# Kernel tuning notes

Measured on AMD Instinct MI355X. Metric: run time of the kernel, lower is better.

The kernel has to match this reference:

```python
import jax, jax.numpy as jnp
import numpy as np

IN_FEATURES = 4096
OUT_FEATURES = 4096
NUM_FRAGMENTS = 32
FRAGMENT_SIZE = IN_FEATURES // NUM_FRAGMENTS  # 128
COMPRESSED = 512
BATCH = 8192


def setup_inputs() -> dict:
    key = jax.random.key(0)
    k_x, k_sel, k_exp, k_c1, k_c2 = jax.random.split(key, 5)
    inv_sqrt_fs = 1.0 / np.sqrt(FRAGMENT_SIZE)
    return {
        "x": jax.random.normal(k_x, (BATCH, IN_FEATURES), dtype=jnp.float32),
        "selector_weights": jax.random.normal(k_sel, (NUM_FRAGMENTS, FRAGMENT_SIZE), dtype=jnp.float32) * inv_sqrt_fs,
        "expert_weights": jax.random.normal(k_exp, (NUM_FRAGMENTS, FRAGMENT_SIZE, OUT_FEATURES), dtype=jnp.float32) * inv_sqrt_fs,
        # store Linear weights as [in, out] so forward is x @ W
        "w_compressor": jax.random.normal(k_c1, (IN_FEATURES, COMPRESSED), dtype=jnp.float32) * (1.0 / np.sqrt(IN_FEATURES)),
        "w_compressed": jax.random.normal(k_c2, (COMPRESSED, OUT_FEATURES), dtype=jnp.float32) * (1.0 / np.sqrt(COMPRESSED)),
    }


def reference(x, selector_weights, expert_weights, w_compressor, w_compressed):
    B, D = x.shape
    F, S = selector_weights.shape  # num_fragments, fragment_size
    x_frag = x.reshape(B, F, S)
    # selector scores and soft routing probs over fragments
    scores = jnp.einsum('bfi,fi->bf', x_frag, selector_weights)
    probs = jax.nn.softmax(scores, axis=1)  # [B, F]
    # soft-routed expert output: weight fragments by probs first to avoid a [B,F,O] intermediate
    x_weighted = x_frag * probs[:, :, None]  # [B, F, S]
    expert_out = jnp.einsum('bfi,fio->bo', x_weighted, expert_weights)  # [B, O]
    # fragment mask mapped to full feature dim: mask = 1 - probs[fragment_mapping]
    mask = 1.0 - jnp.repeat(probs, S, axis=1)  # [B, D]
    masked_input = x * mask
    compressed_out = (masked_input @ w_compressor) @ w_compressed  # [B, O]
    return expert_out + compressed_out
```

## Files before the change

### kernel.cpp

```cpp
#include <hip/hip_runtime.h>
#include <hip/hip_bf16.h>
#include <stdint.h>

#define BATCH 8192
#define IN_F  4096
#define OUT_F 4096
#define NFRAG 32
#define FSIZE 128
#define COMP  512
#define KCAT  4608

typedef float f32x4 __attribute__((ext_vector_type(4)));
typedef short bf16x8 __attribute__((ext_vector_type(8)));

__device__ __forceinline__ unsigned short f2bf(float f) {
  union { float f; unsigned u; } v; v.f = f;
  return (unsigned short)((v.u + 0x7FFFu + ((v.u >> 16) & 1u)) >> 16);
}
__device__ __forceinline__ unsigned pack2(float a, float b) {
  return (unsigned)f2bf(a) | ((unsigned)f2bf(b) << 16);
}

typedef const __attribute__((address_space(1))) unsigned* as1_u32p;
typedef __attribute__((address_space(3))) unsigned* as3_u32p;

__device__ __forceinline__ void lds_load16(const void* g, void* l) {
  __builtin_amdgcn_global_load_lds((as1_u32p)(uintptr_t)g, (as3_u32p)(uintptr_t)l, 16, 0, 0);
}

__global__ __launch_bounds__(256) void k_route(
    const float* __restrict__ x, const float* __restrict__ sel,
    unsigned short* __restrict__ xw, unsigned short* __restrict__ xm) {
  __shared__ float red[256];
  __shared__ float sc[NFRAG];
  const int b = blockIdx.x;
  const int t = threadIdx.x;
  const float* xr = x + (size_t)b * IN_F;
  const int frag = t >> 3;

  float4 v0 = *(const float4*)&xr[t * 16 + 0];
  float4 v1 = *(const float4*)&xr[t * 16 + 4];
  float4 v2 = *(const float4*)&xr[t * 16 + 8];
  float4 v3 = *(const float4*)&xr[t * 16 + 12];
  const float* sw = sel + frag * FSIZE + (t & 7) * 16;
  float4 s0 = *(const float4*)&sw[0];
  float4 s1 = *(const float4*)&sw[4];
  float4 s2 = *(const float4*)&sw[8];
  float4 s3 = *(const float4*)&sw[12];
  float d = v0.x*s0.x + v0.y*s0.y + v0.z*s0.z + v0.w*s0.w
          + v1.x*s1.x + v1.y*s1.y + v1.z*s1.z + v1.w*s1.w
          + v2.x*s2.x + v2.y*s2.y + v2.z*s2.z + v2.w*s2.w
          + v3.x*s3.x + v3.y*s3.y + v3.z*s3.z + v3.w*s3.w;
  red[t] = d;
  __syncthreads();
  if (t < NFRAG) {
    float s = 0.f;
#pragma unroll
    for (int j = 0; j < 8; ++j) s += red[t * 8 + j];
    sc[t] = s;
  }
  __syncthreads();
  float mx = sc[0];
#pragma unroll
  for (int f = 1; f < NFRAG; ++f) mx = fmaxf(mx, sc[f]);
  float den = 0.f;
#pragma unroll
  for (int f = 0; f < NFRAG; ++f) den += __expf(sc[f] - mx);
  const float p = __expf(sc[frag] - mx) / den;
  const float q = 1.f - p;

  const size_t bw = (size_t)b * KCAT + (size_t)t * 16;
  const size_t bm_ = (size_t)b * IN_F + (size_t)t * 16;
  uint4 w;
  w.x = pack2(v0.x*p, v0.y*p); w.y = pack2(v0.z*p, v0.w*p);
  w.z = pack2(v1.x*p, v1.y*p); w.w = pack2(v1.z*p, v1.w*p);
  *(uint4*)&xw[bw] = w;
  w.x = pack2(v2.x*p, v2.y*p); w.y = pack2(v2.z*p, v2.w*p);
  w.z = pack2(v3.x*p, v3.y*p); w.w = pack2(v3.z*p, v3.w*p);
  *(uint4*)&xw[bw + 8] = w;
  w.x = pack2(v0.x*q, v0.y*q); w.y = pack2(v0.z*q, v0.w*q);
  w.z = pack2(v1.x*q, v1.y*q); w.w = pack2(v1.z*q, v1.w*q);
  *(uint4*)&xm[bm_] = w;
  w.x = pack2(v2.x*q, v2.y*q); w.y = pack2(v2.z*q, v2.w*q);
  w.z = pack2(v3.x*q, v3.y*q); w.w = pack2(v3.z*q, v3.w*q);
  *(uint4*)&xm[bm_ + 8] = w;
}

__global__ __launch_bounds__(256) void k_transpose_bf16(
    const float* __restrict__ src, unsigned short* __restrict__ dst,
    int R, int C, int ldd) {
  __shared__ float tile[64][65];
  const int t = threadIdx.x;
  const int c0 = blockIdx.x * 64, r0 = blockIdx.y * 64;
#pragma unroll
  for (int i = 0; i < 4; ++i) {
    const int q = i * 256 + t;
    const int row = q >> 4;
    const int col = (q & 15) << 2;
    float4 v = *(const float4*)&src[(size_t)(r0 + row) * C + c0 + col];
    tile[row][col + 0] = v.x; tile[row][col + 1] = v.y;
    tile[row][col + 2] = v.z; tile[row][col + 3] = v.w;
  }
  __syncthreads();
#pragma unroll
  for (int i = 0; i < 4; ++i) {
    const int q = i * 256 + t;
    const int orow = q >> 4;
    const int oc = (q & 15) << 2;
    ushort4 o;
    o.x = f2bf(tile[oc + 0][orow]);
    o.y = f2bf(tile[oc + 1][orow]);
    o.z = f2bf(tile[oc + 2][orow]);
    o.w = f2bf(tile[oc + 3][orow]);
    *(ushort4*)&dst[(size_t)(c0 + orow) * ldd + r0 + oc] = o;
  }
}

#define BM 128
#define BN 128
#define BK 64

template <int EPI>
__global__ __launch_bounds__(256) void k_gemm_bt(
    const unsigned short* __restrict__ A, int lda,
    const unsigned short* __restrict__ Bt, int ldb,
    void* __restrict__ Cp, int ldc, int M, int N, int K) {
  __shared__ unsigned short lA[BM * BK];
  __shared__ unsigned short lB[BN * BK];
  const int t = threadIdx.x;
  const int lane = t & 63;
  const int wave = t >> 6;
  const int wr = wave >> 1, wc = wave & 1;
  const int hi = lane >> 4, lo = lane & 15;
  const int bm = blockIdx.y * BM, bn = blockIdx.x * BN;

  f32x4 acc[4][4] = {};

  for (int kt = 0; kt < K; kt += BK) {
#pragma unroll
    for (int i = 0; i < 4; ++i) {
      const int c = i * 256 + t;
      const int row = c >> 3, cc = c & 7;
      lds_load16(&A [(size_t)(bm + row) * lda + kt + cc * 8], (char*)lA + c * 16);
      lds_load16(&Bt[(size_t)(bn + row) * ldb + kt + cc * 8], (char*)lB + c * 16);
    }
    __syncthreads();
#pragma unroll
    for (int kk = 0; kk < BK; kk += 32) {
      bf16x8 af[4], bfr[4];
#pragma unroll
      for (int m = 0; m < 4; ++m)
        af[m] = *(const bf16x8*)&lA[(wr * 64 + m * 16 + lo) * BK + kk + hi * 8];
#pragma unroll
      for (int n = 0; n < 4; ++n)
        bfr[n] = *(const bf16x8*)&lB[(wc * 64 + n * 16 + lo) * BK + kk + hi * 8];
#pragma unroll
      for (int m = 0; m < 4; ++m)
#pragma unroll
        for (int n = 0; n < 4; ++n)
          acc[m][n] = __builtin_amdgcn_mfma_f32_16x16x32_bf16(af[m], bfr[n], acc[m][n], 0, 0, 0);
    }
    __syncthreads();
  }

  float* Cf = (float*)Cp;
  unsigned short* Cb = (unsigned short*)Cp;
#pragma unroll
  for (int m = 0; m < 4; ++m)
#pragma unroll
    for (int n = 0; n < 4; ++n)
#pragma unroll
      for (int r = 0; r < 4; ++r) {
        const int row = bm + wr * 64 + m * 16 + hi * 4 + r;
        const int col = bn + wc * 64 + n * 16 + lo;
        const size_t idx = (size_t)row * ldc + col;
        if constexpr (EPI == 0)      Cf[idx] = acc[m][n][r];
        else if constexpr (EPI == 1) Cf[idx] += acc[m][n][r];
        else                         Cb[idx] = f2bf(acc[m][n][r]);
      }
}

#define G_SLOT  16384
#define G_STRIDE 32768
#define G_LDS   98304

__global__ __launch_bounds__(512, 2) void k_gemm256(
    const unsigned short* __restrict__ A, int lda,
    const unsigned short* __restrict__ Bt, int ldb,
    float* __restrict__ C, int M, int N, int K) {
  extern __shared__ char lds[];
  const int t = threadIdx.x;
  const int lane = t & 63;
  const int wid = t >> 6;
  const int wr = wid >> 2;
  const int wc = wid & 3;
  const int lo = lane & 15, hi = lane >> 4;

  const int nwg = gridDim.x;
  const int chunk = nwg >> 3;
  const int remap = ((int)blockIdx.x & 7) * chunk + ((int)blockIdx.x >> 3);
  const int nx = N >> 8;
  const int bm = (remap / nx) << 8;
  const int bn = (remap % nx) << 8;

  const int NT = K >> 5;

  const int c0 = t,       r0 = c0 >> 2, s0 = (c0 & 3) ^ ((r0 >> 1) & 3);
  const int c1 = t + 512, r1 = c1 >> 2, s1 = (c1 & 3) ^ ((r1 >> 1) & 3);
  const unsigned short* Ap0 = A  + (size_t)(bm + r0) * lda + s0 * 8;
  const unsigned short* Ap1 = A  + (size_t)(bm + r1) * lda + s1 * 8;
  const unsigned short* Bp0 = Bt + (size_t)(bn + r0) * ldb + s0 * 8;
  const unsigned short* Bp1 = Bt + (size_t)(bn + r1) * ldb + s1 * 8;

  const int ksl = ((hi ^ ((lo >> 1) & 3)) << 4);
  const int aBase = wr * 8192 + lo * 64 + ksl;
  const int bBase = G_SLOT + wc * 4096 + lo * 64 + ksl;

  f32x4 acc[8][4] = {};

#define STAGE(tt_) do {                                            \
    char* _b = lds + ((tt_) % 3) * G_STRIDE;                       \
    const int _kt = (tt_) << 5;                                    \
    lds_load16(Ap0 + _kt, _b + c0 * 16);                           \
    lds_load16(Ap1 + _kt, _b + c1 * 16);                           \
    lds_load16(Bp0 + _kt, _b + G_SLOT + c0 * 16);                  \
    lds_load16(Bp1 + _kt, _b + G_SLOT + c1 * 16);                  \
  } while (0)

  STAGE(0);
  STAGE(1);
  asm volatile("s_waitcnt vmcnt(4)" ::: "memory");
  __builtin_amdgcn_sched_barrier(0);
  __builtin_amdgcn_s_barrier();
  __builtin_amdgcn_sched_barrier(0);

  for (int tt = 0; tt < NT; ++tt) {
    if (tt + 2 < NT) STAGE(tt + 2);
    __builtin_amdgcn_s_setprio(1);
    const char* sa = lds + (tt % 3) * G_STRIDE;
    bf16x8 a[8], b[4];
#pragma unroll
    for (int n = 0; n < 4; ++n) b[n] = *(const bf16x8*)(sa + bBase + n * 1024);
#pragma unroll
    for (int m = 0; m < 8; ++m) a[m] = *(const bf16x8*)(sa + aBase + m * 1024);
#pragma unroll
    for (int m = 0; m < 8; ++m)
#pragma unroll
      for (int n = 0; n < 4; ++n)
        acc[m][n] = __builtin_amdgcn_mfma_f32_16x16x32_bf16(a[m], b[n], acc[m][n], 0, 0, 0);
    __builtin_amdgcn_s_setprio(0);
    if (tt + 1 < NT) {
      if (tt + 2 < NT) { asm volatile("s_waitcnt vmcnt(4)" ::: "memory"); }
      else             { asm volatile("s_waitcnt vmcnt(0)" ::: "memory"); }
      __builtin_amdgcn_sched_barrier(0);
      __builtin_amdgcn_s_barrier();
      __builtin_amdgcn_sched_barrier(0);
    }
  }
#undef STAGE

#pragma unroll
  for (int m = 0; m < 8; ++m)
#pragma unroll
    for (int n = 0; n < 4; ++n)
#pragma unroll
      for (int r = 0; r < 4; ++r) {
        const int row = bm + wr * 128 + m * 16 + hi * 4 + r;
        const int col = bn + wc * 64 + n * 16 + lo;
        C[(size_t)row * N + col] = acc[m][n][r];
      }
}

extern "C" void kernel_launch(void* const* d_in, const int* in_sizes, int n_in,
                              void* d_out, int out_size, void* d_ws, size_t ws_size,
                              hipStream_t stream) {
  const float* x   = (const float*)d_in[0];
  const float* sel = (const float*)d_in[1];
  const float* ew  = (const float*)d_in[2];
  const float* wc1 = (const float*)d_in[3];
  const float* wc2 = (const float*)d_in[4];
  float* out = (float*)d_out;

  char* ws = (char*)d_ws;
  unsigned short* xcat  = (unsigned short*)(ws);
  unsigned short* xm    = (unsigned short*)(ws + 75497472);
  unsigned short* btcat = (unsigned short*)(ws + 75497472);
  unsigned short* w1ct  = (unsigned short*)(ws + 142606336);

  (void)hipFuncSetAttribute((const void*)k_gemm256,
                            hipFuncAttributeMaxDynamicSharedMemorySize, G_LDS);

  k_route<<<BATCH, 256, 0, stream>>>(x, sel, xcat, xm);
  k_transpose_bf16<<<dim3(COMP / 64, IN_F / 64), 256, 0, stream>>>(wc1, w1ct, IN_F, COMP, IN_F);
  k_gemm_bt<2><<<dim3(COMP / BN, BATCH / BM), 256, 0, stream>>>(
      xm, IN_F, w1ct, IN_F, (void*)(xcat + IN_F), KCAT, BATCH, COMP, IN_F);
  k_transpose_bf16<<<dim3(OUT_F / 64, IN_F / 64), 256, 0, stream>>>(ew, btcat, IN_F, OUT_F, KCAT);
  k_transpose_bf16<<<dim3(OUT_F / 64, COMP / 64), 256, 0, stream>>>(wc2, btcat + IN_F, COMP, OUT_F, KCAT);
  k_gemm256<<<(BATCH / 256) * (OUT_F / 256), 512, G_LDS, stream>>>(
      xcat, KCAT, btcat, KCAT, out, BATCH, OUT_F, KCAT);
}
```

Baseline: 675.3 us.

## Split GEMM main loop into two half-phases interleaving A/B staging with MFMA

Splits each K-iteration of the bf16 GEMM into two phases. Each phase loads half of the A fragments, issues part of the next-next stage global-to-LDS copies (A in one phase, B in the other), synchronises, and runs half of the MFMAs. This is a ping-pong style schedule meant to spread memory issue across the iteration and overlap it better with matrix-core work. It adds four workgroup barriers per iteration instead of one, which costs synchronisation overhead.

```diff
diff --git a/kernel.cpp b/kernel.cpp
--- a/kernel.cpp
+++ b/kernel.cpp
@@ -218,46 +218,68 @@
 
   f32x4 acc[8][4] = {};
 
-#define STAGE(tt_) do {                                            \
+#define STAGE_A(tt_) do {                                          \
     char* _b = lds + ((tt_) % 3) * G_STRIDE;                       \
     const int _kt = (tt_) << 5;                                    \
     lds_load16(Ap0 + _kt, _b + c0 * 16);                           \
     lds_load16(Ap1 + _kt, _b + c1 * 16);                           \
+  } while (0)
+#define STAGE_B(tt_) do {                                          \
+    char* _b = lds + ((tt_) % 3) * G_STRIDE;                       \
+    const int _kt = (tt_) << 5;                                    \
     lds_load16(Bp0 + _kt, _b + G_SLOT + c0 * 16);                  \
     lds_load16(Bp1 + _kt, _b + G_SLOT + c1 * 16);                  \
   } while (0)
 
-  STAGE(0);
-  STAGE(1);
+  STAGE_A(0); STAGE_B(0);
+  STAGE_A(1); STAGE_B(1);
   asm volatile("s_waitcnt vmcnt(4)" ::: "memory");
   __builtin_amdgcn_sched_barrier(0);
   __builtin_amdgcn_s_barrier();
-  __builtin_amdgcn_sched_barrier(0);
 
   for (int tt = 0; tt < NT; ++tt) {
-    if (tt + 2 < NT) STAGE(tt + 2);
-    __builtin_amdgcn_s_setprio(1);
     const char* sa = lds + (tt % 3) * G_STRIDE;
     bf16x8 a[8], b[4];
+
 #pragma unroll
     for (int n = 0; n < 4; ++n) b[n] = *(const bf16x8*)(sa + bBase + n * 1024);
 #pragma unroll
-    for (int m = 0; m < 8; ++m) a[m] = *(const bf16x8*)(sa + aBase + m * 1024);
-#pragma unroll
-    for (int m = 0; m < 8; ++m)
+    for (int m = 0; m < 4; ++m) a[m] = *(const bf16x8*)(sa + aBase + m * 1024);
+    if (tt + 2 < NT) STAGE_A(tt + 2);
+    __builtin_amdgcn_s_barrier();
+    asm volatile("s_waitcnt lgkmcnt(0)" ::: "memory");
+    __builtin_amdgcn_sched_barrier(0);
+    __builtin_amdgcn_s_setprio(1);
+#pragma unroll
+    for (int m = 0; m < 4; ++m)
 #pragma unroll
       for (int n = 0; n < 4; ++n)
         acc[m][n] = __builtin_amdgcn_mfma_f32_16x16x32_bf16(a[m], b[n], acc[m][n], 0, 0, 0);
     __builtin_amdgcn_s_setprio(0);
-    if (tt + 1 < NT) {
-      if (tt + 2 < NT) { asm volatile("s_waitcnt vmcnt(4)" ::: "memory"); }
-      else             { asm volatile("s_waitcnt vmcnt(0)" ::: "memory"); }
-      __builtin_amdgcn_sched_barrier(0);
-      __builtin_amdgcn_s_barrier();
-      __builtin_amdgcn_sched_barrier(0);
+    __builtin_amdgcn_s_barrier();
+
+#pragma unroll
+    for (int m = 4; m < 8; ++m) a[m] = *(const bf16x8*)(sa + aBase + m * 1024);
+    if (tt + 2 < NT) {
+      STAGE_B(tt + 2);
+      asm volatile("s_waitcnt vmcnt(4)" ::: "memory");
+    } else if (tt + 1 < NT) {
+      asm volatile("s_waitcnt vmcnt(0)" ::: "memory");
     }
-  }
-#undef STAGE
+    __builtin_amdgcn_s_barrier();
+    asm volatile("s_waitcnt lgkmcnt(0)" ::: "memory");
+    __builtin_amdgcn_sched_barrier(0);
+    __builtin_amdgcn_s_setprio(1);
+#pragma unroll
+    for (int m = 4; m < 8; ++m)
+#pragma unroll
+      for (int n = 0; n < 4; ++n)
+        acc[m][n] = __builtin_amdgcn_mfma_f32_16x16x32_bf16(a[m], b[n], acc[m][n], 0, 0, 0);
+    __builtin_amdgcn_s_setprio(0);
+    __builtin_amdgcn_s_barrier();
+  }
+#undef STAGE_A
+#undef STAGE_B
 
 #pragma unroll
   for (int m = 0; m < 8; ++m)
```

New measurement: 656.0 us. 2.9% less time.

## Deepen GEMM pipeline to four LDS stages with register double-buffered fragments

Applied to the files above, without the earlier changes.

Grows the LDS ring in the 256x256 bf16 GEMM from three to four stages, prefetching three K-tiles ahead. The main loop is unrolled by two and alternates between two register sets of A/B fragments, so LDS reads for the next tile are issued before the MFMAs of the current tile. Explicit lgkmcnt and vmcnt waits are placed to overlap these reads with MFMA work and with global-to-LDS copies. The goal is to hide LDS read latency behind the matrix cores. The cost is more LDS per block and about 96 extra VGPRs, which risks register spills or lower occupancy.

```diff
diff --git a/kernel.cpp b/kernel.cpp
--- a/kernel.cpp
+++ b/kernel.cpp
@@ -182,7 +182,7 @@
 
 #define G_SLOT  16384
 #define G_STRIDE 32768
-#define G_LDS   98304
+#define G_LDS   131072
 
 __global__ __launch_bounds__(512, 2) void k_gemm256(
     const unsigned short* __restrict__ A, int lda,
@@ -217,9 +217,10 @@
   const int bBase = G_SLOT + wc * 4096 + lo * 64 + ksl;
 
   f32x4 acc[8][4] = {};
+  bf16x8 aR0[8], bR0[4], aR1[8], bR1[4];
 
 #define STAGE(tt_) do {                                            \
-    char* _b = lds + ((tt_) % 3) * G_STRIDE;                       \
+    char* _b = lds + ((tt_) & 3) * G_STRIDE;                       \
     const int _kt = (tt_) << 5;                                    \
     lds_load16(Ap0 + _kt, _b + c0 * 16);                           \
     lds_load16(Ap1 + _kt, _b + c1 * 16);                           \
@@ -227,37 +228,63 @@
     lds_load16(Bp1 + _kt, _b + G_SLOT + c1 * 16);                  \
   } while (0)
 
-  STAGE(0);
-  STAGE(1);
+#define LOADFRAGS(da, db, tt_) do {                                \
+    const char* _s = lds + ((tt_) & 3) * G_STRIDE;                 \
+    _Pragma("unroll")                                              \
+    for (int n = 0; n < 4; ++n) db[n] = *(const bf16x8*)(_s + bBase + n * 1024); \
+    _Pragma("unroll")                                              \
+    for (int m = 0; m < 8; ++m) da[m] = *(const bf16x8*)(_s + aBase + m * 1024); \
+  } while (0)
+
+#define MFMAS(sa_, sb_) do {                                       \
+    _Pragma("unroll")                                              \
+    for (int m = 0; m < 8; ++m)                                    \
+      _Pragma("unroll")                                            \
+      for (int n = 0; n < 4; ++n)                                  \
+        acc[m][n] = __builtin_amdgcn_mfma_f32_16x16x32_bf16(sa_[m], sb_[n], acc[m][n], 0, 0, 0); \
+  } while (0)
+
+  STAGE(0); STAGE(1); STAGE(2);
   asm volatile("s_waitcnt vmcnt(4)" ::: "memory");
   __builtin_amdgcn_sched_barrier(0);
   __builtin_amdgcn_s_barrier();
   __builtin_amdgcn_sched_barrier(0);
-
-  for (int tt = 0; tt < NT; ++tt) {
-    if (tt + 2 < NT) STAGE(tt + 2);
+  LOADFRAGS(aR0, bR0, 0);
+
+  for (int tt = 0; tt < NT; tt += 2) {
+    if (tt + 1 < NT) LOADFRAGS(aR1, bR1, tt + 1);
+    if (tt + 3 < NT) STAGE(tt + 3);
+    if (tt + 1 < NT) { asm volatile("s_waitcnt lgkmcnt(12)" ::: "memory"); }
+    else             { asm volatile("s_waitcnt lgkmcnt(0)"  ::: "memory"); }
+    __builtin_amdgcn_sched_barrier(0);
     __builtin_amdgcn_s_setprio(1);
-    const char* sa = lds + (tt % 3) * G_STRIDE;
-    bf16x8 a[8], b[4];
-#pragma unroll
-    for (int n = 0; n < 4; ++n) b[n] = *(const bf16x8*)(sa + bBase + n * 1024);
-#pragma unroll
-    for (int m = 0; m < 8; ++m) a[m] = *(const bf16x8*)(sa + aBase + m * 1024);
-#pragma unroll
-    for (int m = 0; m < 8; ++m)
-#pragma unroll
-      for (int n = 0; n < 4; ++n)
-        acc[m][n] = __builtin_amdgcn_mfma_f32_16x16x32_bf16(a[m], b[n], acc[m][n], 0, 0, 0);
+    MFMAS(aR0, bR0);
     __builtin_amdgcn_s_setprio(0);
+    if (tt + 3 < NT)      { asm volatile("s_waitcnt vmcnt(4)" ::: "memory"); }
+    else if (tt + 2 < NT) { asm volatile("s_waitcnt vmcnt(0)" ::: "memory"); }
+    __builtin_amdgcn_sched_barrier(0);
+    __builtin_amdgcn_s_barrier();
+    __builtin_amdgcn_sched_barrier(0);
+
     if (tt + 1 < NT) {
-      if (tt + 2 < NT) { asm volatile("s_waitcnt vmcnt(4)" ::: "memory"); }
-      else             { asm volatile("s_waitcnt vmcnt(0)" ::: "memory"); }
+      if (tt + 2 < NT) LOADFRAGS(aR0, bR0, tt + 2);
+      if (tt + 4 < NT) STAGE(tt + 4);
+      if (tt + 2 < NT) { asm volatile("s_waitcnt lgkmcnt(12)" ::: "memory"); }
+      else             { asm volatile("s_waitcnt lgkmcnt(0)"  ::: "memory"); }
+      __builtin_amdgcn_sched_barrier(0);
+      __builtin_amdgcn_s_setprio(1);
+      MFMAS(aR1, bR1);
+      __builtin_amdgcn_s_setprio(0);
+      if (tt + 4 < NT)      { asm volatile("s_waitcnt vmcnt(4)" ::: "memory"); }
+      else if (tt + 3 < NT) { asm volatile("s_waitcnt vmcnt(0)" ::: "memory"); }
       __builtin_amdgcn_sched_barrier(0);
       __builtin_amdgcn_s_barrier();
       __builtin_amdgcn_sched_barrier(0);
     }
   }
 #undef STAGE
+#undef LOADFRAGS
+#undef MFMAS
 
 #pragma unroll
   for (int m = 0; m < 8; ++m)
```

After: 671.0 us. Within noise of the previous version (-0.6%).
